# Kernel tuning notes

Hardware: AMD Instinct MI355X
Metric: run time of the kernel (lower is better)

Reference implementation:

```python
import jax, jax.numpy as jnp
import numpy as np

N, D, DOUT = 10000, 128, 128
KS, KN, KC, NCENTER, HID = 32, 16, 16, 3, 32  # HID = D // 4


def setup_inputs() -> dict:
    key = jax.random.key(0)
    ks = jax.random.split(key, 32)
    p = lambda i, shape: jax.random.normal(ks[i], shape, dtype=jnp.float32) * 0.05
    return {
        "ids": jnp.arange(N, dtype=jnp.int64) if jax.config.jax_enable_x64 else jnp.arange(N, dtype=jnp.int32),
        "feats": jax.random.normal(ks[0], (N, D), dtype=jnp.float32),
        "cluster_idx": jax.random.randint(ks[1], (N, NCENTER, KC), 0, N),
        "struct_idx": jax.random.randint(ks[2], (N, KS), 0, N),
        "epo": 100,
        # VertexConv (cluster): Transform convKK grouped conv -> (k,k,D) weight, (k,k) bias; convK1 -> (k,) weight, scalar bias
        "wKK_c": p(3, (KC, KC, D)), "bKK_c": p(4, (KC, KC)), "wK1_c": p(5, (KC,)), "bK1_c": p(6, ()),
        # VertexConv (knn)
        "wKK_n": p(7, (KN, KN, D)), "bKK_n": p(8, (KN, KN)), "wK1_n": p(9, (KN,)), "bK1_n": p(10, ()),
        # VertexConv (structure)
        "wKK_s": p(11, (KS, KS, D)), "bKK_s": p(12, (KS, KS)), "wK1_s": p(13, (KS,)), "bK1_s": p(14, ()),
        # EdgeConv attention MLP: Linear(D, D//4) -> ReLU -> Linear(D//4, 1)
        "ec_w1": p(15, (D, HID)), "ec_b1": p(16, (HID,)), "ec_w2": p(17, (HID,)), "ec_b2": p(18, ()),
        # Final Linear(D, DOUT)
        "fc_w": p(19, (D, DOUT)), "fc_b": p(20, (DOUT,)),
    }


def vertex_conv(x, wKK, bKK, wK1, bK1):
    # x: (N, k, d). Grouped Conv1d(k, k*k, d, groups=k): mult[n,i,j] = <wKK[i,j], x[n,i]> + bKK[i,j]
    mult = jnp.einsum("nid,ijd->nij", x, wKK) + bKK
    mult = jax.nn.softmax(mult, axis=-1)                 # softmax over last dim
    transformed = jnp.einsum("nij,njd->nid", mult, x)    # (N, k, d)
    # Conv1d(k, 1, 1): weighted sum over the k channels
    return jnp.einsum("nkd,k->nd", transformed, wK1) + bK1


def reference(ids, feats, cluster_idx, struct_idx, epo,
              wKK_c, bKK_c, wK1_c, bK1_c,
              wKK_n, bKK_n, wK1_n, bK1_n,
              wKK_s, bKK_s, wK1_s, bK1_s,
              ec_w1, ec_b1, ec_w2, ec_b2, fc_w, fc_b):
    # epo=100 >= all warmups -> all three hyperedge branches active (static).
    # --- cluster hyperedges (precomputed kmeans index table) ---
    c_feats = feats[cluster_idx[ids]]                    # (N, n_center, kc, d)
    hyperedge = [vertex_conv(c_feats[:, c], wKK_c, bKK_c, wK1_c, bK1_c)
                 for c in range(NCENTER)]
    # --- knn hyperedge: cosine similarity + topk (cos_dis) ---
    nrm = jnp.maximum(jnp.linalg.norm(feats, axis=1, keepdims=True), 1e-12)
    xn = feats / nrm
    sim = xn @ xn.T                                      # (N, N) -- memory-dominant
    _, knn_idx = jax.lax.top_k(sim, KN)                  # (N, kn)
    hyperedge.append(vertex_conv(feats[knn_idx[ids]], wKK_n, bKK_n, wK1_n, bK1_n))
    # --- structure hyperedge (precomputed sampled edge_dict table) ---
    hyperedge.append(vertex_conv(feats[struct_idx[ids]], wKK_s, bKK_s, wK1_s, bK1_s))
    x = jnp.stack(hyperedge, axis=1)                     # (N, t, d), t = n_center + 2
    # EdgeConv: MLP attention over the t hyperedges, softmax along t, weighted sum
    h = jax.nn.relu(jnp.einsum("ntd,dh->nth", x, ec_w1) + ec_b1)
    scores = jax.nn.softmax(jnp.einsum("nth,h->nt", h, ec_w2) + ec_b2, axis=1)
    agg = jnp.einsum("nt,ntd->nd", scores, x)            # (N, d)
    # final fc + relu (dropout = identity in eval)
    return jax.nn.relu(agg @ fc_w + fc_b)
```

## Files before the change

### kernel.cpp

```cpp
#include <hip/hip_runtime.h>
#include <cmath>


#define N_NODES 10000
#define D 128
#define DQ 32
#define NCB 3
#define T_HE 5
#define HID_SZ 32
#define NCH 16
#define CHUNK 625
#define TOPK 16
#define TOPM 32

typedef __attribute__((ext_vector_type(8))) short short8;
typedef __attribute__((ext_vector_type(8))) _Float16 half8;
typedef __attribute__((ext_vector_type(4))) float f32x4;
typedef __attribute__((ext_vector_type(16))) float f32x16;

__device__ __forceinline__ unsigned bf16rne(float f) {
  unsigned u = __float_as_uint(f);
  return (u + 0x7FFFu + ((u >> 16) & 1u)) >> 16;
}

__global__ __launch_bounds__(256) void kpre(const float* __restrict__ feats,
                                            const float* __restrict__ wc,
                                            const float* __restrict__ wn,
                                            const float* __restrict__ wstr,
                                            unsigned short* __restrict__ xnh,
                                            _Float16* __restrict__ fH16,
                                            double* __restrict__ normD,
                                            _Float16* __restrict__ wH16) {
  int bx = blockIdx.x;
  int tid = threadIdx.x;
  if (bx < 2500) {
    int n = bx * 4 + (tid >> 6);
    int lane = tid & 63;
    float2 v = ((const float2*)(feats + (size_t)n * D))[lane];
    _Float16 p2[2] = {(_Float16)v.x, (_Float16)v.y};
    ((unsigned*)(fH16 + (size_t)n * D))[lane] = *(const unsigned*)p2;
    double ss = (double)v.x * (double)v.x + (double)v.y * (double)v.y;
#pragma unroll
    for (int o = 32; o > 0; o >>= 1) ss += __shfl_xor(ss, o);
    double nd = fmax(sqrt(ss), 1e-12);
    if (lane == 0) normD[n] = nd;
    float inv = (float)(1.0 / nd);
    ((unsigned*)(xnh + (size_t)n * D))[lane] = bf16rne(v.x * inv) | (bf16rne(v.y * inv) << 16);
  } else {
    int p = (bx - 2500) * 256 + tid;
    if (p >= 98304) return;
    int e = p * 2;
    float2 v;
    if (e < 32768) v = *(const float2*)(wc + e);
    else if (e < 65536) v = *(const float2*)(wn + (e - 32768));
    else v = *(const float2*)(wstr + (e - 65536));
    _Float16 p2[2] = {(_Float16)v.x, (_Float16)v.y};
    ((unsigned*)wH16)[p] = *(const unsigned*)p2;
  }
}

__device__ __forceinline__ void ceu(unsigned& a, unsigned& b) {
  unsigned lo = min(a, b), hi = max(a, b);
  a = lo; b = hi;
}
__device__ __forceinline__ void ceu64(unsigned long long& a, unsigned long long& b) {
  unsigned long long lo = min(a, b), hi = max(a, b);
  a = lo; b = hi;
}
__device__ __forceinline__ void sort16_asc(unsigned (&v)[16]) {
#pragma unroll
  for (int k = 2; k <= 16; k <<= 1) {
#pragma unroll
    for (int j = k >> 1; j > 0; j >>= 1) {
#pragma unroll
      for (int i = 0; i < 16; i++) {
        int x = i ^ j;
        if (x > i) {
          if ((i & k) == 0) ceu(v[i], v[x]);
          else ceu(v[x], v[i]);
        }
      }
    }
  }
}
__device__ __forceinline__ void merge16_asc(unsigned (&run)[16], const unsigned (&b)[16]) {
  unsigned m[16];
#pragma unroll
  for (int i = 0; i < 16; i++) m[i] = max(run[i], b[15 - i]);
#pragma unroll
  for (int j = 8; j > 0; j >>= 1) {
#pragma unroll
    for (int i = 0; i < 16; i++) {
      if ((i & j) == 0) ceu(m[i], m[i + j]);
    }
  }
#pragma unroll
  for (int i = 0; i < 16; i++) run[i] = m[i];
}

__device__ __forceinline__ void vc16_body(int tid, int n0, int tslot,
    int* idxLm, float* coefPm, float* coefSm,
    const _Float16* __restrict__ fH16, const _Float16* __restrict__ wH16,
    const int* __restrict__ idxTab, int istr, int ioff, int woff,
    const float* __restrict__ bKK, const float* __restrict__ wK1,
    const float* __restrict__ bK1p, float* __restrict__ hx) {
  int w = tid >> 6, lane = tid & 63, l15 = lane & 15, quad = lane >> 4;
  const half8* fH = (const half8*)fH16;
  {
    int nn = tid >> 4, i = tid & 15;
    idxLm[nn * 33 + i] = idxTab[(size_t)(n0 + nn) * istr + ioff + i];
  }
  __syncthreads();
  const half8* wHv = (const half8*)(wH16 + woff);
  f32x4 coef = {0.f, 0.f, 0.f, 0.f};
#pragma unroll
  for (int ii = 0; ii < 4; ii++) {
    int i = w * 4 + ii;
    int rowi = idxLm[l15 * 33 + i];
    float bkk = bKK[i * 16 + l15];
    f32x4 acc = {0.f, 0.f, 0.f, 0.f};
#pragma unroll
    for (int kc = 0; kc < 4; kc++) {
      half8 ah = fH[(size_t)rowi * 16 + kc * 4 + quad];
      half8 bh = wHv[((size_t)i * 16 + l15) * 16 + kc * 4 + quad];
      acc = __builtin_amdgcn_mfma_f32_16x16x32_f16(ah, bh, acc, 0, 0, 0);
    }
    float wki = wK1[i];
#pragma unroll
    for (int r = 0; r < 4; r++) {
      float v = acc[r] + bkk;
      float mx = v;
#pragma unroll
      for (int msk = 1; msk < 16; msk <<= 1) mx = fmaxf(mx, __shfl_xor(mx, msk));
      float e = __expf(v - mx);
      float s = e;
#pragma unroll
      for (int msk = 1; msk < 16; msk <<= 1) s += __shfl_xor(s, msk);
      coef[r] += wki * (e / s);
    }
  }
#pragma unroll
  for (int r = 0; r < 4; r++) coefPm[(w * 16 + quad * 4 + r) * 33 + l15] = coef[r];
  __syncthreads();
  {
    int nn = tid >> 4, j = tid & 15;
    coefSm[nn * 33 + j] = coefPm[(nn) * 33 + j] + coefPm[(16 + nn) * 33 + j] +
                          coefPm[(32 + nn) * 33 + j] + coefPm[(48 + nn) * 33 + j];
  }
  __syncthreads();
  {
    int nl = tid >> 4, g = tid & 15;
    float bk1 = bK1p[0];
    float a8[8];
#pragma unroll
    for (int t = 0; t < 8; t++) a8[t] = bk1;
    for (int j = 0; j < 16; j++) {
      float cf = coefSm[nl * 33 + j];
      int rowj = idxLm[nl * 33 + j];
      half8 xv = fH[(size_t)rowj * 16 + g];
#pragma unroll
      for (int e = 0; e < 8; e++) a8[e] = fmaf(cf, (float)xv[e], a8[e]);
    }
    int node = n0 + nl;
    float4* o = (float4*)(hx + ((size_t)node * T_HE + tslot) * D + g * 8);
    o[0] = make_float4(a8[0], a8[1], a8[2], a8[3]);
    o[1] = make_float4(a8[4], a8[5], a8[6], a8[7]);
  }
}

__device__ __forceinline__ void vc32_body(int tid, int n0,
    int* idxLm, float* coefPm, float* coefSm,
    const _Float16* __restrict__ fH16, const _Float16* __restrict__ wH16,
    const int* __restrict__ struct_idx,
    const float* __restrict__ bKK_s, const float* __restrict__ wK1_s,
    const float* __restrict__ bK1_s, float* __restrict__ hx) {
  int w = tid >> 6, lane = tid & 63, l15 = lane & 15, quad = lane >> 4;
  const half8* fH = (const half8*)fH16;
  for (int e = tid; e < 512; e += 256) {
    int nn = e >> 5, i = e & 31;
    idxLm[nn * 33 + i] = struct_idx[(size_t)(n0 + nn) * 32 + i];
  }
  __syncthreads();
  const half8* wHv = (const half8*)(wH16 + 65536);
  f32x4 coef0 = {0.f, 0.f, 0.f, 0.f};
  f32x4 coef1 = {0.f, 0.f, 0.f, 0.f};
#pragma unroll
  for (int ii = 0; ii < 8; ii++) {
    int i = w * 8 + ii;
    int rowi = idxLm[l15 * 33 + i];
    float bk0 = bKK_s[i * 32 + l15];
    float bk1v = bKK_s[i * 32 + 16 + l15];
    f32x4 a0 = {0.f, 0.f, 0.f, 0.f};
    f32x4 a1 = {0.f, 0.f, 0.f, 0.f};
#pragma unroll
    for (int kc = 0; kc < 4; kc++) {
      half8 ah = fH[(size_t)rowi * 16 + kc * 4 + quad];
      half8 b0 = wHv[((size_t)i * 32 + l15) * 16 + kc * 4 + quad];
      half8 b1 = wHv[((size_t)i * 32 + 16 + l15) * 16 + kc * 4 + quad];
      a0 = __builtin_amdgcn_mfma_f32_16x16x32_f16(ah, b0, a0, 0, 0, 0);
      a1 = __builtin_amdgcn_mfma_f32_16x16x32_f16(ah, b1, a1, 0, 0, 0);
    }
    float wki = wK1_s[i];
#pragma unroll
    for (int r = 0; r < 4; r++) {
      float v0 = a0[r] + bk0, v1 = a1[r] + bk1v;
      float mx = fmaxf(v0, v1);
#pragma unroll
      for (int msk = 1; msk < 16; msk <<= 1) mx = fmaxf(mx, __shfl_xor(mx, msk));
      float e0 = __expf(v0 - mx), e1 = __expf(v1 - mx);
      float s = e0 + e1;
#pragma unroll
      for (int msk = 1; msk < 16; msk <<= 1) s += __shfl_xor(s, msk);
      float inv = wki / s;
      coef0[r] += e0 * inv;
      coef1[r] += e1 * inv;
    }
  }
#pragma unroll
  for (int r = 0; r < 4; r++) {
    coefPm[(w * 16 + quad * 4 + r) * 33 + l15] = coef0[r];
    coefPm[(w * 16 + quad * 4 + r) * 33 + l15 + 16] = coef1[r];
  }
  __syncthreads();
  for (int e = tid; e < 512; e += 256) {
    int nn = e >> 5, j = e & 31;
    coefSm[nn * 33 + j] = coefPm[nn * 33 + j] + coefPm[(16 + nn) * 33 + j] +
                          coefPm[(32 + nn) * 33 + j] + coefPm[(48 + nn) * 33 + j];
  }
  __syncthreads();
  {
    int nl = tid >> 4, g = tid & 15;
    float bk1 = bK1_s[0];
    float a8[8];
#pragma unroll
    for (int t = 0; t < 8; t++) a8[t] = bk1;
    for (int j = 0; j < 32; j++) {
      float cf = coefSm[nl * 33 + j];
      int rowj = idxLm[nl * 33 + j];
      half8 xv = fH[(size_t)rowj * 16 + g];
#pragma unroll
      for (int e = 0; e < 8; e++) a8[e] = fmaf(cf, (float)xv[e], a8[e]);
    }
    int node = n0 + nl;
    float4* o = (float4*)(hx + ((size_t)node * T_HE + 4) * D + g * 8);
    o[0] = make_float4(a8[0], a8[1], a8[2], a8[3]);
    o[1] = make_float4(a8[4], a8[5], a8[6], a8[7]);
  }
}

__global__ __launch_bounds__(256, 4) void ksimvc(
    const unsigned short* __restrict__ xnh, unsigned* __restrict__ cand,
    const _Float16* __restrict__ fH16, const _Float16* __restrict__ wH16,
    const int* __restrict__ cluster_idx, const int* __restrict__ struct_idx,
    const float* __restrict__ bKK_c, const float* __restrict__ bKK_s,
    const float* __restrict__ wK1_c, const float* __restrict__ bK1_c,
    const float* __restrict__ wK1_s, const float* __restrict__ bK1_s,
    float* __restrict__ hx) {
  __shared__ __align__(16) unsigned char smem[32768];
  int bx = blockIdx.x;
  int tid = threadIdx.x;
  int r3 = bx % 3, q3 = bx / 3;
  if (r3 == 0) {
    short* Bb = (short*)smem;
    int rb = q3 % 79, chunk = q3 / 79;
    int w = tid >> 6, lane = tid & 63, l31 = lane & 31, lh = lane >> 5;
    int row0 = rb * 128 + w * 32;
    int cbase = chunk * CHUNK;

    short8 afr[8];
    {
      int ar = min(row0 + l31, N_NODES - 1);
      const short8* ap = (const short8*)(xnh + (size_t)ar * D);
#pragma unroll
      for (int ks = 0; ks < 8; ks++) afr[ks] = ap[ks * 2 + lh];
    }

    unsigned run[16];
#pragma unroll
    for (int s = 0; s < 16; s++) run[s] = 0u;

    for (int ti = 0; ti < 5; ti++) {
      int tb = cbase + ti * 128;
      __syncthreads();
      {
        int ci = tid >> 1, h = tid & 1;
        int gcol = min(tb + ci, N_NODES - 1);
        const short8* gp = (const short8*)(xnh + (size_t)gcol * D);
        short8* bp = (short8*)Bb;
#pragma unroll
        for (int i = 0; i < 8; i++) bp[(h * 8 + i) * 128 + ci] = gp[h * 8 + i];
      }
      __syncthreads();

      const short8* bv = (const short8*)Bb;
#pragma unroll
      for (int half = 0; half < 2; half++) {
        f32x16 acc[2];
#pragma unroll
        for (int nj = 0; nj < 2; nj++)
#pragma unroll
          for (int r = 0; r < 16; r++) acc[nj][r] = 0.f;
#pragma unroll
        for (int ks = 0; ks < 8; ks++) {
          int kp = ks * 2 + lh;
#pragma unroll
          for (int nj = 0; nj < 2; nj++) {
            int ni = half * 2 + nj;
            short8 af = bv[kp * 128 + ni * 32 + l31];
            acc[nj] = __builtin_amdgcn_mfma_f32_32x32x16_bf16(af, afr[ks], acc[nj], 0, 0, 0);
          }
        }
#pragma unroll
        for (int nj = 0; nj < 2; nj++) {
          int ni = half * 2 + nj;
          unsigned bt[16];
#pragma unroll
          for (int reg = 0; reg < 16; reg++) {
            int m = (reg & 3) + 8 * (reg >> 2) + 4 * lh;
            int cic = ti * 128 + ni * 32 + m;
            unsigned bb = __float_as_uint(acc[nj][reg]);
            unsigned mu = (bb & 0x80000000u) ? ~bb : (bb | 0x80000000u);
            bt[reg] = (cic < CHUNK) ? ((mu & 0xFFFFFC00u) | (unsigned)(1023 - cic)) : 0u;
          }
          sort16_asc(bt);
          merge16_asc(run, bt);
        }
      }
    }
    {
      unsigned other[16];
#pragma unroll
      for (int s = 0; s < 16; s++) other[s] = (unsigned)__shfl_xor((int)run[s], 32);
      merge16_asc(run, other);
    }
    int grow = row0 + l31;
    if (lh == 0 && grow < N_NODES) {
      unsigned* o = cand + ((size_t)grow * NCH + chunk) * 16;
#pragma unroll
      for (int i = 0; i < 16; i += 4)
        *(uint4*)(o + i) = make_uint4(run[i], run[i + 1], run[i + 2], run[i + 3]);
    }
  } else {
    int vid = q3 * 2 + (r3 - 1);
    if (vid >= 2500) return;
    int zz = vid / 625, bi = vid - zz * 625;
    int n0 = bi * 16;
    int* idxLm = (int*)smem;
    float* coefPm = (float*)(smem + 2112);
    float* coefSm = (float*)(smem + 10560);
    if (zz < 3) {
      vc16_body(tid, n0, zz, idxLm, coefPm, coefSm, fH16, wH16,
                cluster_idx, NCB * 16, zz * 16, 0, bKK_c, wK1_c, bK1_c, hx);
    } else {
      vc32_body(tid, n0, idxLm, coefPm, coefSm, fH16, wH16,
                struct_idx, bKK_s, wK1_s, bK1_s, hx);
    }
  }
}

__global__ __launch_bounds__(256, 4) void kvc3(
    const _Float16* __restrict__ fH16, const _Float16* __restrict__ wH16,
    const int* __restrict__ knn,
    const float* __restrict__ bKK_n, const float* __restrict__ wK1_n,
    const float* __restrict__ bK1_n, float* __restrict__ hx) {
  __shared__ __align__(16) unsigned char smem[12672];
  int* idxLm = (int*)smem;
  float* coefPm = (float*)(smem + 2112);
  float* coefSm = (float*)(smem + 10560);
  vc16_body(threadIdx.x, blockIdx.x * 16, 3, idxLm, coefPm, coefSm, fH16, wH16,
            knn, 16, 0, 32768, bKK_n, wK1_n, bK1_n, hx);
}

__global__ __launch_bounds__(64) void kmerge(const unsigned* __restrict__ cand,
                                             int* __restrict__ candIdx) {
  int row = blockIdx.x * 64 + threadIdx.x;
  if (row >= N_NODES) return;
  unsigned long long run[TOPM];
#pragma unroll
  for (int s = 0; s < TOPM; s++) run[s] = 0ull;
  const uint4* c4 = (const uint4*)(cand + (size_t)row * (NCH * 16));
  for (int ch = 0; ch < NCH; ch++) {
    unsigned b[16];
#pragma unroll
    for (int q = 0; q < 4; q++) {
      uint4 t = c4[ch * 4 + q];
      b[q * 4 + 0] = t.x; b[q * 4 + 1] = t.y;
      b[q * 4 + 2] = t.z; b[q * 4 + 3] = t.w;
    }
    unsigned base = (unsigned)(ch * CHUNK);
    unsigned long long b64[16];
#pragma unroll
    for (int s = 0; s < 16; s++) {
      unsigned k = b[s];
      unsigned gcol = base + (1023u - (k & 1023u));
      b64[s] = ((unsigned long long)(k >> 10) << 32) | (unsigned long long)(~gcol);
    }
#pragma unroll
    for (int i = 0; i < 16; i++) run[i] = max(run[i], b64[15 - i]);
#pragma unroll
    for (int j = 16; j > 0; j >>= 1)
#pragma unroll
      for (int i = 0; i < TOPM; i++)
        if ((i & j) == 0) ceu64(run[i], run[i + j]);
  }
  int4* o4 = (int4*)(candIdx + (size_t)row * TOPM);
#pragma unroll
  for (int s = 0; s < TOPM; s += 4) {
    int4 o;
    o.x = (int)(~(unsigned)(run[s + 0] & 0xFFFFFFFFull));
    o.y = (int)(~(unsigned)(run[s + 1] & 0xFFFFFFFFull));
    o.z = (int)(~(unsigned)(run[s + 2] & 0xFFFFFFFFull));
    o.w = (int)(~(unsigned)(run[s + 3] & 0xFFFFFFFFull));
    o4[s >> 2] = o;
  }
}

__global__ __launch_bounds__(256) void krerank(const float* __restrict__ feats,
                                               const double* __restrict__ normD,
                                               const int* __restrict__ candIdx,
                                               int* __restrict__ knn) {
  __shared__ float rowF[D];
  __shared__ double simL[TOPM];
  __shared__ int idxL[TOPM];
  int row = blockIdx.x;
  int tid = threadIdx.x;
  if (tid < DQ)
    ((float4*)rowF)[tid] = ((const float4*)(feats + (size_t)row * D))[tid];
  int c = tid >> 3, part = tid & 7;
  int cnd = candIdx[(size_t)row * TOPM + c];
  __syncthreads();
  const float4* f4 = (const float4*)(feats + (size_t)cnd * D);
  double acc = 0.0;
#pragma unroll
  for (int g = 0; g < 4; g++) {
    float4 v = f4[part * 4 + g];
    const float* rf = &rowF[(part * 4 + g) * 4];
    acc = fma((double)v.x, (double)rf[0], acc);
    acc = fma((double)v.y, (double)rf[1], acc);
    acc = fma((double)v.z, (double)rf[2], acc);
    acc = fma((double)v.w, (double)rf[3], acc);
  }
  acc += __shfl_down(acc, 4);
  acc += __shfl_down(acc, 2);
  acc += __shfl_down(acc, 1);
  if (part == 0) {
    simL[c] = acc / (normD[row] * normD[cnd]);
    idxL[c] = cnd;
  }
  __syncthreads();
  if (tid < TOPM) {
    double s = simL[tid];
    int idx = idxL[tid];
    int rank = 0;
#pragma unroll
    for (int o = 0; o < TOPM; o++) {
      double so = simL[o];
      int io = idxL[o];
      rank += (so > s || (so == s && io < idx)) ? 1 : 0;
    }
    if (rank < TOPK) knn[(size_t)row * TOPK + rank] = idx;
  }
}

__global__ __launch_bounds__(256) void kfinal(const float* __restrict__ hx,
    const float* __restrict__ w1, const float* __restrict__ b1,
    const float* __restrict__ w2, const float* __restrict__ b2p,
    const float* __restrict__ fcw, const float* __restrict__ fcb,
    float* __restrict__ out) {
  __shared__ float xL[8][T_HE][D];
  __shared__ float hL[8][T_HE][HID_SZ];
  __shared__ float scL[8][T_HE];
  __shared__ float aggL[8][D];
  int tid = threadIdx.x;
  int n0 = blockIdx.x * 8;
  const float4* hx4 = (const float4*)hx;
  for (int q = tid; q < 8 * T_HE * DQ; q += 256) {
    int nn = q / (T_HE * DQ);
    int rem = q - nn * (T_HE * DQ);
    int t = rem / DQ;
    int dq = rem & 31;
    int node = n0 + nn;
    float4 val = make_float4(0.f, 0.f, 0.f, 0.f);
    if (node < N_NODES) val = hx4[((size_t)node * T_HE + t) * DQ + dq];
    *(float4*)&xL[nn][t][dq << 2] = val;
  }
  __syncthreads();
  for (int q = tid; q < 8 * T_HE * HID_SZ; q += 256) {
    int nn = q / (T_HE * HID_SZ);
    int rem = q - nn * (T_HE * HID_SZ);
    int t = rem / HID_SZ;
    int hh = rem & (HID_SZ - 1);
    float acc = b1[hh];
    const float4* xv4 = (const float4*)xL[nn][t];
    for (int dq = 0; dq < 32; dq++) {
      float4 xv = xv4[dq];
      int db = dq * 4;
      acc = fmaf(xv.x, w1[(db + 0) * HID_SZ + hh], acc);
      acc = fmaf(xv.y, w1[(db + 1) * HID_SZ + hh], acc);
      acc = fmaf(xv.z, w1[(db + 2) * HID_SZ + hh], acc);
      acc = fmaf(xv.w, w1[(db + 3) * HID_SZ + hh], acc);
    }
    hL[nn][t][hh] = fmaxf(acc, 0.f);
  }
  __syncthreads();
  if (tid < 8 * T_HE) {
    int nn = tid / T_HE, t = tid % T_HE;
    float acc = b2p[0];
    for (int hh = 0; hh < HID_SZ; hh++) acc = fmaf(hL[nn][t][hh], w2[hh], acc);
    scL[nn][t] = acc;
  }
  __syncthreads();
  if (tid < 8) {
    float mx = -1e30f;
#pragma unroll
    for (int t = 0; t < T_HE; t++) mx = fmaxf(mx, scL[tid][t]);
    float e[T_HE];
    float s = 0.f;
#pragma unroll
    for (int t = 0; t < T_HE; t++) { e[t] = expf(scL[tid][t] - mx); s += e[t]; }
    float inv = 1.f / s;
#pragma unroll
    for (int t = 0; t < T_HE; t++) scL[tid][t] = e[t] * inv;
  }
  __syncthreads();
  {
    int nn = tid >> 5, dq = tid & 31;
    float4 acc = make_float4(0.f, 0.f, 0.f, 0.f);
#pragma unroll
    for (int t = 0; t < T_HE; t++) {
      float sw = scL[nn][t];
      float4 xv = *(const float4*)&xL[nn][t][dq << 2];
      acc.x = fmaf(sw, xv.x, acc.x);
      acc.y = fmaf(sw, xv.y, acc.y);
      acc.z = fmaf(sw, xv.z, acc.z);
      acc.w = fmaf(sw, xv.w, acc.w);
    }
    *(float4*)&aggL[nn][dq << 2] = acc;
  }
  __syncthreads();
  {
    int dout = tid & 127, g = tid >> 7;
    float a0 = fcb[dout], a1 = a0, a2 = a0, a3 = a0;
    for (int dq = 0; dq < 32; dq++) {
      int db = dq * 4;
      float wv0 = fcw[(db + 0) * 128 + dout];
      float wv1 = fcw[(db + 1) * 128 + dout];
      float wv2 = fcw[(db + 2) * 128 + dout];
      float wv3 = fcw[(db + 3) * 128 + dout];
      float4 v0 = *(const float4*)&aggL[g * 4 + 0][db];
      float4 v1 = *(const float4*)&aggL[g * 4 + 1][db];
      float4 v2 = *(const float4*)&aggL[g * 4 + 2][db];
      float4 v3 = *(const float4*)&aggL[g * 4 + 3][db];
      a0 = fmaf(v0.x, wv0, fmaf(v0.y, wv1, fmaf(v0.z, wv2, fmaf(v0.w, wv3, a0))));
      a1 = fmaf(v1.x, wv0, fmaf(v1.y, wv1, fmaf(v1.z, wv2, fmaf(v1.w, wv3, a1))));
      a2 = fmaf(v2.x, wv0, fmaf(v2.y, wv1, fmaf(v2.z, wv2, fmaf(v2.w, wv3, a2))));
      a3 = fmaf(v3.x, wv0, fmaf(v3.y, wv1, fmaf(v3.z, wv2, fmaf(v3.w, wv3, a3))));
    }
    int nb = n0 + g * 4;
    if (nb + 0 < N_NODES) out[(size_t)(nb + 0) * 128 + dout] = fmaxf(a0, 0.f);
    if (nb + 1 < N_NODES) out[(size_t)(nb + 1) * 128 + dout] = fmaxf(a1, 0.f);
    if (nb + 2 < N_NODES) out[(size_t)(nb + 2) * 128 + dout] = fmaxf(a2, 0.f);
    if (nb + 3 < N_NODES) out[(size_t)(nb + 3) * 128 + dout] = fmaxf(a3, 0.f);
  }
}

extern "C" void kernel_launch(void* const* d_in, const int* in_sizes, int n_in,
                              void* d_out, int out_size, void* d_ws, size_t ws_size,
                              hipStream_t stream) {
  (void)in_sizes; (void)n_in; (void)out_size; (void)ws_size;
  const float* feats       = (const float*)d_in[1];
  const int*   cluster_idx = (const int*)d_in[2];
  const int*   struct_idx  = (const int*)d_in[3];
  const float* wKK_c = (const float*)d_in[5];
  const float* bKK_c = (const float*)d_in[6];
  const float* wK1_c = (const float*)d_in[7];
  const float* bK1_c = (const float*)d_in[8];
  const float* wKK_n = (const float*)d_in[9];
  const float* bKK_n = (const float*)d_in[10];
  const float* wK1_n = (const float*)d_in[11];
  const float* bK1_n = (const float*)d_in[12];
  const float* wKK_s = (const float*)d_in[13];
  const float* bKK_s = (const float*)d_in[14];
  const float* wK1_s = (const float*)d_in[15];
  const float* bK1_s = (const float*)d_in[16];
  const float* ec_w1 = (const float*)d_in[17];
  const float* ec_b1 = (const float*)d_in[18];
  const float* ec_w2 = (const float*)d_in[19];
  const float* ec_b2 = (const float*)d_in[20];
  const float* fc_w  = (const float*)d_in[21];
  const float* fc_b  = (const float*)d_in[22];
  float* out = (float*)d_out;

  char* wsb = (char*)d_ws;
  unsigned short* xnh = (unsigned short*)(wsb);
  unsigned* cand = (unsigned*)(wsb + 2560000);
  int* candIdx = (int*)(wsb + 12800000);
  double* normD = (double*)(wsb + 14080000);
  _Float16* fH16 = (_Float16*)(wsb + 14160000);
  _Float16* wH16 = (_Float16*)(wsb + 16720000);
  int* knnIdx = (int*)(wsb + 46080000);
  float* hx = (float*)(wsb + 46720000);

  kpre<<<2884, 256, 0, stream>>>(feats, wKK_c, wKK_n, wKK_s,
                                 xnh, fH16, normD, wH16);
  ksimvc<<<3792, 256, 0, stream>>>(xnh, cand, fH16, wH16, cluster_idx, struct_idx,
                                   bKK_c, bKK_s, wK1_c, bK1_c, wK1_s, bK1_s, hx);
  kmerge<<<(N_NODES + 63) / 64, 64, 0, stream>>>(cand, candIdx);
  krerank<<<N_NODES, 256, 0, stream>>>(feats, normD, candIdx, knnIdx);
  kvc3<<<625, 256, 0, stream>>>(fH16, wH16, knnIdx, bKK_n, wK1_n, bK1_n, hx);
  kfinal<<<1250, 256, 0, stream>>>(hx, ec_w1, ec_b1, ec_w2, ec_b2, fc_w, fc_b, out);
}
```

Before: 367.1 us.

## Rebalance similarity chunks, use cheaper sort network and simplified positive key encoding

Cuts the similarity column range into 20 chunks of 500 (4 tiles each) instead of 16 of 625, which removes the partially wasted fifth tile, and changes how similarity and vertex-conv blocks interleave in the grid. It replaces the 16-element bitonic sort with Batcher's odd-even merge sort, which uses fewer compare-exchanges. The accumulators now start at 2.0 so every cosine score is positive, letting the raw float bits serve as the sort key without sign flipping, with a 9-bit column index. It also packs the workspace layout more tightly. The risks are lost key precision from the extra truncated mantissa bit and tie ordering changing from lowest to highest index, which the rerank stage must absorb.

```diff
diff --git a/kernel.cpp b/kernel.cpp
--- a/kernel.cpp
+++ b/kernel.cpp
@@ -8,8 +8,9 @@
 #define NCB 3
 #define T_HE 5
 #define HID_SZ 32
-#define NCH 16
-#define CHUNK 625
+#define NCH 20
+#define CHUNK 500
+#define TPC 4
 #define TOPK 16
 #define TOPM 32
 
@@ -67,21 +68,21 @@
   unsigned long long lo = min(a, b), hi = max(a, b);
   a = lo; b = hi;
 }
-__device__ __forceinline__ void sort16_asc(unsigned (&v)[16]) {
-#pragma unroll
-  for (int k = 2; k <= 16; k <<= 1) {
-#pragma unroll
-    for (int j = k >> 1; j > 0; j >>= 1) {
-#pragma unroll
-      for (int i = 0; i < 16; i++) {
-        int x = i ^ j;
-        if (x > i) {
-          if ((i & k) == 0) ceu(v[i], v[x]);
-          else ceu(v[x], v[i]);
-        }
-      }
-    }
-  }
+__device__ __forceinline__ void oems16_asc(unsigned (&v)[16]) {
+  ceu(v[0], v[1]); ceu(v[2], v[3]); ceu(v[0], v[2]); ceu(v[1], v[3]); ceu(v[1], v[2]);
+  ceu(v[4], v[5]); ceu(v[6], v[7]); ceu(v[4], v[6]); ceu(v[5], v[7]); ceu(v[5], v[6]);
+  ceu(v[0], v[4]); ceu(v[2], v[6]); ceu(v[2], v[4]); ceu(v[1], v[5]); ceu(v[3], v[7]);
+  ceu(v[3], v[5]); ceu(v[1], v[2]); ceu(v[3], v[4]); ceu(v[5], v[6]);
+  ceu(v[8], v[9]); ceu(v[10], v[11]); ceu(v[8], v[10]); ceu(v[9], v[11]); ceu(v[9], v[10]);
+  ceu(v[12], v[13]); ceu(v[14], v[15]); ceu(v[12], v[14]); ceu(v[13], v[15]); ceu(v[13], v[14]);
+  ceu(v[8], v[12]); ceu(v[10], v[14]); ceu(v[10], v[12]); ceu(v[9], v[13]); ceu(v[11], v[15]);
+  ceu(v[11], v[13]); ceu(v[9], v[10]); ceu(v[11], v[12]); ceu(v[13], v[14]);
+  ceu(v[0], v[8]); ceu(v[4], v[12]); ceu(v[4], v[8]); ceu(v[2], v[10]); ceu(v[6], v[14]);
+  ceu(v[6], v[10]); ceu(v[2], v[4]); ceu(v[6], v[8]); ceu(v[10], v[12]);
+  ceu(v[1], v[9]); ceu(v[5], v[13]); ceu(v[5], v[9]); ceu(v[3], v[11]); ceu(v[7], v[15]);
+  ceu(v[7], v[11]); ceu(v[3], v[5]); ceu(v[7], v[9]); ceu(v[11], v[13]);
+  ceu(v[1], v[2]); ceu(v[3], v[4]); ceu(v[5], v[6]); ceu(v[7], v[8]); ceu(v[9], v[10]);
+  ceu(v[11], v[12]); ceu(v[13], v[14]);
 }
 __device__ __forceinline__ void merge16_asc(unsigned (&run)[16], const unsigned (&b)[16]) {
   unsigned m[16];
@@ -259,10 +260,17 @@
   __shared__ __align__(16) unsigned char smem[32768];
   int bx = blockIdx.x;
   int tid = threadIdx.x;
-  int r3 = bx % 3, q3 = bx / 3;
-  if (r3 == 0) {
+  int sid = -1, vid = -1;
+  if (bx < 3950) {
+    int g = bx / 5, r = bx - g * 5;
+    if (r < 2) sid = g * 2 + r;
+    else vid = g * 3 + (r - 2);
+  } else {
+    vid = 2370 + (bx - 3950);
+  }
+  if (sid >= 0) {
     short* Bb = (short*)smem;
-    int rb = q3 % 79, chunk = q3 / 79;
+    int rb = sid % 79, chunk = sid / 79;
     int w = tid >> 6, lane = tid & 63, l31 = lane & 31, lh = lane >> 5;
     int row0 = rb * 128 + w * 32;
     int cbase = chunk * CHUNK;
@@ -279,7 +287,7 @@
 #pragma unroll
     for (int s = 0; s < 16; s++) run[s] = 0u;
 
-    for (int ti = 0; ti < 5; ti++) {
+    for (int ti = 0; ti < TPC; ti++) {
       int tb = cbase + ti * 128;
       __syncthreads();
       {
@@ -299,7 +307,7 @@
 #pragma unroll
         for (int nj = 0; nj < 2; nj++)
 #pragma unroll
-          for (int r = 0; r < 16; r++) acc[nj][r] = 0.f;
+          for (int r = 0; r < 16; r++) acc[nj][r] = 2.0f;
 #pragma unroll
         for (int ks = 0; ks < 8; ks++) {
           int kp = ks * 2 + lh;
@@ -319,10 +327,17 @@
             int m = (reg & 3) + 8 * (reg >> 2) + 4 * lh;
             int cic = ti * 128 + ni * 32 + m;
             unsigned bb = __float_as_uint(acc[nj][reg]);
-            unsigned mu = (bb & 0x80000000u) ? ~bb : (bb | 0x80000000u);
-            bt[reg] = (cic < CHUNK) ? ((mu & 0xFFFFFC00u) | (unsigned)(1023 - cic)) : 0u;
+            bt[reg] = (bb & 0xFFFFFE00u) | (unsigned)cic;
           }
-          sort16_asc(bt);
+          if (ti == TPC - 1) {
+#pragma unroll
+            for (int reg = 0; reg < 16; reg++) {
+              int m = (reg & 3) + 8 * (reg >> 2) + 4 * lh;
+              int off = ni * 32 + m;
+              if (off >= CHUNK - (TPC - 1) * 128) bt[reg] = 0u;
+            }
+          }
+          oems16_asc(bt);
           merge16_asc(run, bt);
         }
       }
@@ -341,8 +356,6 @@
         *(uint4*)(o + i) = make_uint4(run[i], run[i + 1], run[i + 2], run[i + 3]);
     }
   } else {
-    int vid = q3 * 2 + (r3 - 1);
-    if (vid >= 2500) return;
     int zz = vid / 625, bi = vid - zz * 625;
     int n0 = bi * 16;
     int* idxLm = (int*)smem;
@@ -392,8 +405,8 @@
 #pragma unroll
     for (int s = 0; s < 16; s++) {
       unsigned k = b[s];
-      unsigned gcol = base + (1023u - (k & 1023u));
-      b64[s] = ((unsigned long long)(k >> 10) << 32) | (unsigned long long)(~gcol);
+      unsigned gcol = base + (k & 511u);
+      b64[s] = ((unsigned long long)(k >> 9) << 32) | (unsigned long long)gcol;
     }
 #pragma unroll
     for (int i = 0; i < 16; i++) run[i] = max(run[i], b64[15 - i]);
@@ -407,10 +420,10 @@
 #pragma unroll
   for (int s = 0; s < TOPM; s += 4) {
     int4 o;
-    o.x = (int)(~(unsigned)(run[s + 0] & 0xFFFFFFFFull));
-    o.y = (int)(~(unsigned)(run[s + 1] & 0xFFFFFFFFull));
-    o.z = (int)(~(unsigned)(run[s + 2] & 0xFFFFFFFFull));
-    o.w = (int)(~(unsigned)(run[s + 3] & 0xFFFFFFFFull));
+    o.x = (int)(unsigned)(run[s + 0] & 0xFFFFFFFFull);
+    o.y = (int)(unsigned)(run[s + 1] & 0xFFFFFFFFull);
+    o.z = (int)(unsigned)(run[s + 2] & 0xFFFFFFFFull);
+    o.w = (int)(unsigned)(run[s + 3] & 0xFFFFFFFFull);
     o4[s >> 2] = o;
   }
 }
@@ -593,17 +606,17 @@
 
   char* wsb = (char*)d_ws;
   unsigned short* xnh = (unsigned short*)(wsb);
-  unsigned* cand = (unsigned*)(wsb + 2560000);
-  int* candIdx = (int*)(wsb + 12800000);
-  double* normD = (double*)(wsb + 14080000);
-  _Float16* fH16 = (_Float16*)(wsb + 14160000);
-  _Float16* wH16 = (_Float16*)(wsb + 16720000);
-  int* knnIdx = (int*)(wsb + 46080000);
-  float* hx = (float*)(wsb + 46720000);
+  _Float16* fH16 = (_Float16*)(wsb + 2560000);
+  _Float16* wH16 = (_Float16*)(wsb + 5120000);
+  double* normD = (double*)(wsb + 5513216);
+  unsigned* cand = (unsigned*)(wsb + 5593216);
+  int* candIdx = (int*)(wsb + 18393216);
+  int* knnIdx = (int*)(wsb + 19673216);
+  float* hx = (float*)(wsb + 20313216);
 
   kpre<<<2884, 256, 0, stream>>>(feats, wKK_c, wKK_n, wKK_s,
                                  xnh, fH16, normD, wH16);
-  ksimvc<<<3792, 256, 0, stream>>>(xnh, cand, fH16, wH16, cluster_idx, struct_idx,
+  ksimvc<<<4080, 256, 0, stream>>>(xnh, cand, fH16, wH16, cluster_idx, struct_idx,
                                    bKK_c, bKK_s, wK1_c, bK1_c, wK1_s, bK1_s, hx);
   kmerge<<<(N_NODES + 63) / 64, 64, 0, stream>>>(cand, candIdx);
   krerank<<<N_NODES, 256, 0, stream>>>(feats, normD, candIdx, knnIdx);
```

New measurement: 385.9 us. 1.05x slower.
